# Kernel tuning notes

Hardware: AMD Instinct MI355X
Metric: run time of the kernel (lower is better)

The kernel has to match this reference:

```python
import jax, jax.numpy as jnp
import numpy as np

B, T, P, D, H = 4, 12, 196, 512, 8
DH = D // H
EPS = 1e-6


def _norm(x, alpha, bias):
    # torch Norm: alpha*(x-mean)/(std_unbiased+eps)+bias, std uses Bessel correction (ddof=1)
    mu = jnp.mean(x, axis=-1, keepdims=True)
    sd = jnp.std(x, axis=-1, ddof=1, keepdims=True)
    return alpha * (x - mu) / (sd + EPS) + bias


def setup_inputs() -> dict:
    key = jax.random.key(0)
    ks = jax.random.split(key, 12)
    s = 0.02

    def n(k, shape, scale=s):
        return jax.random.normal(k, shape, jnp.float32) * scale

    return {
        "x": jax.random.normal(ks[0], (B, T, P, D), jnp.float32),
        "Wq": n(ks[1], (D, D)), "bq": jnp.zeros((D,), jnp.float32),
        "Wk": n(ks[2], (D, D)), "bk": jnp.zeros((D,), jnp.float32),
        "Wv": n(ks[3], (D, D)), "bv": jnp.zeros((D,), jnp.float32),
        "in_a": jnp.ones((D,), jnp.float32), "in_b": jnp.zeros((D,), jnp.float32),
        "attn_a": jnp.ones((D,), jnp.float32), "attn_b": jnp.zeros((D,), jnp.float32),
        "out_a": jnp.ones((D,), jnp.float32), "out_b": jnp.zeros((D,), jnp.float32),
        "Wt": n(ks[4], (T, D, D)), "bt": jnp.zeros((T, D), jnp.float32),
        "pos": n(ks[5], (T, T, P, D), 0.02),
        "W1": n(ks[6], (2 * D, D)), "b1": jnp.zeros((2 * D,), jnp.float32),
        "W2": n(ks[7], (D, 2 * D)), "b2": jnp.zeros((D,), jnp.float32),
    }


def reference(x, Wq, bq, Wk, bk, Wv, bv, in_a, in_b, attn_a, attn_b,
              out_a, out_b, Wt, bt, pos, W1, b1, W2, b2):
    x2 = _norm(x, in_a, in_b)

    def proj(W, b):
        # [B,T,P,D] -> [B,T,H,P,DH]
        return (x2 @ W.T + b).reshape(B, T, P, H, DH).transpose(0, 1, 3, 2, 4)

    Q = proj(Wq, bq)
    K = proj(Wk, bk)
    V = proj(Wv, bv)

    # all-pairs temporal cross attention: [B,t,u,H,Pq,Pk]
    qk = jnp.einsum('btijk,builk->btuijl', Q, K) / np.sqrt(DH)
    attn = jax.nn.softmax(qk, axis=-1)  # no mask, dropout=0
    av = jnp.einsum('btuijl,builk->btuijk', attn, V)  # [B,t,u,H,P,DH]
    av = av.transpose(0, 1, 2, 4, 3, 5).reshape(B, T, T, P, D)
    av = _norm(av, attn_a, attn_b)
    x2p = av + pos  # pos broadcasts over batch

    # per-u Linear fused as one batched contraction, summed over u
    tc = jnp.einsum('btupd,ued->btpe', x2p / T, Wt) + jnp.sum(bt, axis=0)
    x = x + jax.nn.gelu(tc, approximate=False)

    x2 = _norm(x, out_a, out_b)
    h = jax.nn.gelu(x2 @ W1.T + b1, approximate=False)
    y = jax.nn.gelu(h @ W2.T + b2, approximate=False)
    return x + y
```

## Files before the change

### kernel.cpp

```cpp
#include <hip/hip_runtime.h>
#include <hip/hip_bf16.h>

typedef __hip_bfloat16 bf16;

typedef __bf16 bfrag8 __attribute__((ext_vector_type(8)));
typedef __bf16 bfrag4 __attribute__((ext_vector_type(4)));
typedef float  ffrag4 __attribute__((ext_vector_type(4)));
typedef float  ffrag16 __attribute__((ext_vector_type(16)));

#define EPS 1e-6f

__device__ __forceinline__ float gelu_exact(float v) {
  return 0.5f * v * (1.0f + erff(v * 0.7071067811865475f));
}

__device__ __forceinline__ void async16(const void* g, void* s) {
  __builtin_amdgcn_global_load_lds(
      (const __attribute__((address_space(1))) unsigned int*)g,
      (__attribute__((address_space(3))) unsigned int*)s, 16, 0, 0);
}

__device__ __forceinline__ int cvt_pk_bf16(float a, float b) {
  int r;
  asm("v_cvt_pk_bf16_f32 %0, %1, %2" : "=v"(r) : "v"(a), "v"(b));
  return r;
}
__device__ __forceinline__ void perm_swap(int& a, int& b) {
  asm volatile("v_permlane32_swap_b32 %0, %1" : "+v"(a), "+v"(b));
}

struct alignas(16) bf16x8 { bf16 v[8]; };
struct alignas(4)  bf16p2 { __bf16 v[2]; };

__global__ __launch_bounds__(256) void conv_w_kernel(
    const float* __restrict__ Wq, const float* __restrict__ Wk,
    const float* __restrict__ Wv, const float* __restrict__ W1,
    const float* __restrict__ W2, const float* __restrict__ Wt,
    __bf16* __restrict__ dst)
{
  size_t e = ((size_t)blockIdx.x * 256 + threadIdx.x) * 8;
  const float* src; size_t off, dsto;
  if      (e <  262144) { src = Wq; off = e;           dsto = e; }
  else if (e <  524288) { src = Wk; off = e -  262144; dsto = e; }
  else if (e <  786432) { src = Wv; off = e -  524288; dsto = e; }
  else if (e < 1310720) { src = W1; off = e -  786432; dsto = e; }
  else if (e < 1835008) { src = W2; off = e - 1310720; dsto = e; }
  else if (e < 4980736) {
    src = Wt; off = e - 1835008;
    size_t u = off >> 18;
    size_t rem = off & 262143;
    size_t eo = rem >> 9, d = rem & 511;
    dsto = 1835008 + eo * 6144 + u * 512 + d;
  }
  else return;
  float4 f0 = *(const float4*)(src + off);
  float4 f1 = *(const float4*)(src + off + 4);
  bfrag8 o;
  o[0] = (__bf16)f0.x; o[1] = (__bf16)f0.y; o[2] = (__bf16)f0.z; o[3] = (__bf16)f0.w;
  o[4] = (__bf16)f1.x; o[5] = (__bf16)f1.y; o[6] = (__bf16)f1.z; o[7] = (__bf16)f1.w;
  *(bfrag8*)(dst + dsto) = o;
}

__global__ __launch_bounds__(512) void sum_bt_kernel(
    const float* __restrict__ bt, float* __restrict__ sbt)
{
  int n = threadIdx.x;
  float s = 0.f;
#pragma unroll
  for (int u = 0; u < 12; ++u) s += bt[u * 512 + n];
  sbt[n] = s;
}

__global__ __launch_bounds__(64) void norm_f32_to_bf16_kernel(
    const float* __restrict__ in, __bf16* __restrict__ out,
    const float* __restrict__ alpha, const float* __restrict__ beta)
{
  size_t row = blockIdx.x;
  int l = threadIdx.x;
  const float* r = in + row * 512 + l * 8;
  float4 v0 = *(const float4*)(r);
  float4 v1 = *(const float4*)(r + 4);
  float f[8] = {v0.x, v0.y, v0.z, v0.w, v1.x, v1.y, v1.z, v1.w};
  float s = 0.f, ss = 0.f;
#pragma unroll
  for (int q = 0; q < 8; ++q) { s += f[q]; ss += f[q] * f[q]; }
#pragma unroll
  for (int off = 32; off; off >>= 1) { s += __shfl_xor(s, off); ss += __shfl_xor(ss, off); }
  float mu = s * (1.f / 512.f);
  float var = fmaxf((ss - 512.f * mu * mu) * (1.f / 511.f), 0.f);
  float inv = 1.f / (sqrtf(var) + EPS);
  const float* al = alpha + l * 8;
  const float* be = beta + l * 8;
  float4 a0 = *(const float4*)al, a1 = *(const float4*)(al + 4);
  float4 b0 = *(const float4*)be, b1 = *(const float4*)(be + 4);
  float aa[8] = {a0.x, a0.y, a0.z, a0.w, a1.x, a1.y, a1.z, a1.w};
  float bb[8] = {b0.x, b0.y, b0.z, b0.w, b1.x, b1.y, b1.z, b1.w};
  bfrag8 o;
#pragma unroll
  for (int q = 0; q < 8; ++q) o[q] = (__bf16)(aa[q] * (f[q] - mu) * inv + bb[q]);
  *(bfrag8*)(out + row * 512 + l * 8) = o;
}

__global__ __launch_bounds__(256) void norm_av_kernel(
    bf16* __restrict__ av, const float* __restrict__ alpha,
    const float* __restrict__ beta, const float* __restrict__ pos)
{
  size_t row = (size_t)blockIdx.x * 4 + (threadIdx.x >> 6);
  int l = threadIdx.x & 63;
  bf16* r = av + row * 512 + (size_t)l * 8;
  bf16x8 ib = *(const bf16x8*)r;
  float f[8];
#pragma unroll
  for (int q = 0; q < 8; ++q) f[q] = __bfloat162float(ib.v[q]);
  float s = 0.f, ss = 0.f;
#pragma unroll
  for (int q = 0; q < 8; ++q) { s += f[q]; ss += f[q] * f[q]; }
#pragma unroll
  for (int off = 32; off; off >>= 1) { s += __shfl_xor(s, off); ss += __shfl_xor(ss, off); }
  float mu = s * (1.f / 512.f);
  float var = fmaxf((ss - 512.f * mu * mu) * (1.f / 511.f), 0.f);
  float inv = 1.f / (sqrtf(var) + EPS);
  size_t prow = row % 28224;
  const float* pr = pos + prow * 512 + l * 8;
  float4 p0 = *(const float4*)pr, p1 = *(const float4*)(pr + 4);
  const float* al = alpha + l * 8;
  const float* be = beta + l * 8;
  float4 a0 = *(const float4*)al, a1 = *(const float4*)(al + 4);
  float4 b0 = *(const float4*)be, b1 = *(const float4*)(be + 4);
  float pa[8] = {p0.x, p0.y, p0.z, p0.w, p1.x, p1.y, p1.z, p1.w};
  float aa[8] = {a0.x, a0.y, a0.z, a0.w, a1.x, a1.y, a1.z, a1.w};
  float bb[8] = {b0.x, b0.y, b0.z, b0.w, b1.x, b1.y, b1.z, b1.w};
  bf16x8 ob;
#pragma unroll
  for (int q = 0; q < 8; ++q)
    ob.v[q] = __float2bfloat16(aa[q] * (f[q] - mu) * inv + bb[q] + pa[q]);
  *(bf16x8*)r = ob;
}

__global__ __launch_bounds__(256) void mfma_nt_kernel(
    const __bf16* __restrict__ A,
    const __bf16* __restrict__ Bq, const __bf16* __restrict__ Bk,
    const __bf16* __restrict__ Bv,
    const float* __restrict__ bq, const float* __restrict__ bk,
    const float* __restrict__ bv,
    __bf16* __restrict__ oq, __bf16* __restrict__ ok, __bf16* __restrict__ ov,
    const float* __restrict__ res, float* __restrict__ fout,
    int K, int mode)
{
  __shared__ __bf16 As[3 * 128 * 32];
  __shared__ __bf16 Bs[3 * 128 * 32];
  int tid = threadIdx.x;

  int nwg = gridDim.x * gridDim.y;
  int cpx = nwg >> 3;
  int lid = blockIdx.x + gridDim.x * blockIdx.y;
  int logical = (lid & 7) * cpx + (lid >> 3);
  int bx = logical % gridDim.x;
  int by = logical / gridDim.x;
  int m0 = by * 128;
  int n0g = bx * 128;

  const __bf16* Bsel; const float* biassel; __bf16* osel; int ncol0;
  if (mode == 0) {
    int sel = n0g >> 9;
    Bsel = sel == 0 ? Bq : (sel == 1 ? Bk : Bv);
    biassel = sel == 0 ? bq : (sel == 1 ? bk : bv);
    osel = sel == 0 ? oq : (sel == 1 ? ok : ov);
    ncol0 = n0g & 511;
  } else {
    Bsel = Bq; biassel = bq; osel = oq; ncol0 = n0g;
  }

  int srow = tid >> 2;
  int scol = ((tid & 3) ^ ((srow >> 1) & 3)) * 8;
  int rg0 = m0 + srow;       if (rg0 > 9407) rg0 = 9407;
  int rg1 = m0 + 64 + srow;  if (rg1 > 9407) rg1 = 9407;
  const __bf16* a0 = A + (size_t)rg0 * K + scol;
  const __bf16* a1 = A + (size_t)rg1 * K + scol;
  const __bf16* b0 = Bsel + (size_t)(ncol0 + srow) * K + scol;
  const __bf16* b1 = Bsel + (size_t)(ncol0 + 64 + srow) * K + scol;
  char* sa0 = (char*)As + tid * 16;
  char* sa1 = (char*)As + 4096 + tid * 16;
  char* sb0 = (char*)Bs + tid * 16;
  char* sb1 = (char*)Bs + 4096 + tid * 16;

  int l = tid & 63, w = tid >> 6;
  int lm = l & 15, lq = l >> 4;
  int wm = w >> 1, wn = w & 1;
  int rsw = ((((lm >> 1) & 3) ^ lq)) * 8;

  const int nsteps = K >> 5;
  async16(a0, sa0); async16(a1, sa1);
  async16(b0, sb0); async16(b1, sb1);
  async16(a0 + 32, sa0 + 8192); async16(a1 + 32, sa1 + 8192);
  async16(b0 + 32, sb0 + 8192); async16(b1 + 32, sb1 + 8192);
  __builtin_amdgcn_sched_barrier(0);
  asm volatile("s_waitcnt vmcnt(4)" ::: "memory");
  __builtin_amdgcn_s_barrier();
  __builtin_amdgcn_sched_barrier(0);

  ffrag4 acc[4][4] = {};
  int cur = 0;
  for (int t = 0; t < nsteps; ++t) {
    if (t + 2 < nsteps) {
      int k2 = (t + 2) << 5;
      int nb = cur + 2; if (nb >= 3) nb -= 3;
      int bo = nb * 8192;
      async16(a0 + k2, sa0 + bo); async16(a1 + k2, sa1 + bo);
      async16(b0 + k2, sb0 + bo); async16(b1 + k2, sb1 + bo);
    }
    int co = cur * 4096;
    bfrag8 af[4], bfr[4];
#pragma unroll
    for (int i = 0; i < 4; ++i)
      af[i] = *(const bfrag8*)&As[co + (wm * 64 + i * 16 + lm) * 32 + rsw];
#pragma unroll
    for (int j = 0; j < 4; ++j)
      bfr[j] = *(const bfrag8*)&Bs[co + (wn * 64 + j * 16 + lm) * 32 + rsw];
#pragma unroll
    for (int i = 0; i < 4; ++i)
#pragma unroll
      for (int j = 0; j < 4; ++j)
        acc[i][j] = __builtin_amdgcn_mfma_f32_16x16x32_bf16(af[i], bfr[j], acc[i][j], 0, 0, 0);
    __builtin_amdgcn_sched_barrier(0);
    if (t + 2 < nsteps) asm volatile("s_waitcnt vmcnt(4)" ::: "memory");
    else                asm volatile("s_waitcnt vmcnt(0)" ::: "memory");
    __builtin_amdgcn_s_barrier();
    __builtin_amdgcn_sched_barrier(0);
    cur += 1; if (cur == 3) cur = 0;
  }

#pragma unroll
  for (int i = 0; i < 4; ++i) {
    int mbase = m0 + wm * 64 + i * 16 + lq * 4;
#pragma unroll
    for (int j = 0; j < 4; ++j) {
      int n = ncol0 + wn * 64 + j * 16 + lm;
      float bj = biassel[n];
#pragma unroll
      for (int r = 0; r < 4; ++r) {
        int mr = mbase + r;
        if (mr < 9408) {
          float v = acc[i][j][r] + bj;
          if (mode == 0)      osel[(size_t)mr * 512 + n] = (__bf16)v;
          else if (mode == 1) osel[(size_t)mr * 1024 + n] = (__bf16)gelu_exact(v);
          else                fout[(size_t)mr * 512 + n] =
                                res[(size_t)mr * 512 + n] + gelu_exact(v);
        }
      }
    }
  }
}

__global__ __launch_bounds__(256) void mfma_tc_kernel(
    const __bf16* __restrict__ X2p, const __bf16* __restrict__ Wte,
    float* __restrict__ acc0, float* __restrict__ acc1)
{
  __shared__ __bf16 As[3 * 128 * 32];
  __shared__ __bf16 Bs[3 * 128 * 32];
  int tid = threadIdx.x;

  int lid = blockIdx.x + 4 * (blockIdx.y + 74 * blockIdx.z);
  int logical = (lid & 7) * 74 + (lid >> 3);
  int lx = logical & 3;
  int rest = logical >> 2;
  int ly = rest % 74;
  int lz = rest / 74;

  int m0 = ly * 128;
  int n0 = lx * 128;
  int kbeg = lz * 3072;
  float* accp = lz == 0 ? acc0 : acc1;

  int srow = tid >> 2;
  int scol = ((tid & 3) ^ ((srow >> 1) & 3)) * 8;
  int rg0 = m0 + srow;       if (rg0 > 9407) rg0 = 9407;
  int rg1 = m0 + 64 + srow;  if (rg1 > 9407) rg1 = 9407;
  int btq0 = rg0 / 196, p0_ = rg0 - btq0 * 196;
  int btq1 = rg1 / 196, p1_ = rg1 - btq1 * 196;
  const __bf16* a0 = X2p + (size_t)btq0 * 1204224 + (size_t)p0_ * 512 + scol;
  const __bf16* a1 = X2p + (size_t)btq1 * 1204224 + (size_t)p1_ * 512 + scol;
  const __bf16* b0 = Wte + (size_t)(n0 + srow) * 6144 + scol;
  const __bf16* b1 = Wte + (size_t)(n0 + 64 + srow) * 6144 + scol;
  char* sa0 = (char*)As + tid * 16;
  char* sa1 = (char*)As + 4096 + tid * 16;
  char* sb0 = (char*)Bs + tid * 16;
  char* sb1 = (char*)Bs + 4096 + tid * 16;

  int l = tid & 63, w = tid >> 6;
  int lm = l & 15, lq = l >> 4;
  int wm = w >> 1, wn = w & 1;
  int rsw = ((((lm >> 1) & 3) ^ lq)) * 8;

  {
    size_t ao0 = (size_t)(kbeg >> 9) * 100352 + (size_t)(kbeg & 511);
    int k1 = kbeg + 32;
    size_t ao1 = (size_t)(k1 >> 9) * 100352 + (size_t)(k1 & 511);
    async16(a0 + ao0, sa0); async16(a1 + ao0, sa1);
    async16(b0 + kbeg, sb0); async16(b1 + kbeg, sb1);
    async16(a0 + ao1, sa0 + 8192); async16(a1 + ao1, sa1 + 8192);
    async16(b0 + k1, sb0 + 8192); async16(b1 + k1, sb1 + 8192);
  }
  __builtin_amdgcn_sched_barrier(0);
  asm volatile("s_waitcnt vmcnt(4)" ::: "memory");
  __builtin_amdgcn_s_barrier();
  __builtin_amdgcn_sched_barrier(0);

  ffrag4 acc[4][4] = {};
  int cur = 0;
  for (int t = 0; t < 96; ++t) {
    if (t + 2 < 96) {
      int k2 = kbeg + (t + 2) * 32;
      size_t aoff = (size_t)(k2 >> 9) * 100352 + (size_t)(k2 & 511);
      int nb = cur + 2; if (nb >= 3) nb -= 3;
      int bo = nb * 8192;
      async16(a0 + aoff, sa0 + bo); async16(a1 + aoff, sa1 + bo);
      async16(b0 + k2, sb0 + bo); async16(b1 + k2, sb1 + bo);
    }
    int co = cur * 4096;
    bfrag8 af[4], bfr[4];
#pragma unroll
    for (int i = 0; i < 4; ++i)
      af[i] = *(const bfrag8*)&As[co + (wm * 64 + i * 16 + lm) * 32 + rsw];
#pragma unroll
    for (int j = 0; j < 4; ++j)
      bfr[j] = *(const bfrag8*)&Bs[co + (wn * 64 + j * 16 + lm) * 32 + rsw];
#pragma unroll
    for (int i = 0; i < 4; ++i)
#pragma unroll
      for (int j = 0; j < 4; ++j)
        acc[i][j] = __builtin_amdgcn_mfma_f32_16x16x32_bf16(af[i], bfr[j], acc[i][j], 0, 0, 0);
    __builtin_amdgcn_sched_barrier(0);
    if (t + 2 < 96) asm volatile("s_waitcnt vmcnt(4)" ::: "memory");
    else            asm volatile("s_waitcnt vmcnt(0)" ::: "memory");
    __builtin_amdgcn_s_barrier();
    __builtin_amdgcn_sched_barrier(0);
    cur += 1; if (cur == 3) cur = 0;
  }

#pragma unroll
  for (int i = 0; i < 4; ++i) {
    int mbase = m0 + wm * 64 + i * 16 + lq * 4;
#pragma unroll
    for (int j = 0; j < 4; ++j) {
      int n = n0 + wn * 64 + j * 16 + lm;
#pragma unroll
      for (int r = 0; r < 4; ++r) {
        int mr = mbase + r;
        if (mr < 9408)
          accp[(size_t)mr * 512 + n] = acc[i][j][r];
      }
    }
  }
}

__global__ __launch_bounds__(64) void tc_epi_norm_kernel(
    const float* __restrict__ acc0, const float* __restrict__ acc1,
    const float* __restrict__ x, const float* __restrict__ sbt,
    const float* __restrict__ alpha, const float* __restrict__ beta,
    float* __restrict__ xmid, __bf16* __restrict__ x3b)
{
  size_t row = blockIdx.x;
  int l = threadIdx.x;
  size_t base = row * 512 + l * 8;
  float4 c0 = *(const float4*)(acc0 + base);
  float4 c1 = *(const float4*)(acc0 + base + 4);
  float4 d0 = *(const float4*)(acc1 + base);
  float4 d1 = *(const float4*)(acc1 + base + 4);
  float4 x0 = *(const float4*)(x + base);
  float4 x1 = *(const float4*)(x + base + 4);
  float4 s0 = *(const float4*)(sbt + l * 8);
  float4 s1 = *(const float4*)(sbt + l * 8 + 4);
  float cc[8] = {c0.x + d0.x, c0.y + d0.y, c0.z + d0.z, c0.w + d0.w,
                 c1.x + d1.x, c1.y + d1.y, c1.z + d1.z, c1.w + d1.w};
  float xx[8] = {x0.x, x0.y, x0.z, x0.w, x1.x, x1.y, x1.z, x1.w};
  float sv[8] = {s0.x, s0.y, s0.z, s0.w, s1.x, s1.y, s1.z, s1.w};
  float f[8];
#pragma unroll
  for (int q = 0; q < 8; ++q)
    f[q] = xx[q] + gelu_exact(cc[q] * (1.f / 12.f) + sv[q]);
  *(float4*)(xmid + base)     = make_float4(f[0], f[1], f[2], f[3]);
  *(float4*)(xmid + base + 4) = make_float4(f[4], f[5], f[6], f[7]);
  float s = 0.f, ss = 0.f;
#pragma unroll
  for (int q = 0; q < 8; ++q) { s += f[q]; ss += f[q] * f[q]; }
#pragma unroll
  for (int off = 32; off; off >>= 1) { s += __shfl_xor(s, off); ss += __shfl_xor(ss, off); }
  float mu = s * (1.f / 512.f);
  float var = fmaxf((ss - 512.f * mu * mu) * (1.f / 511.f), 0.f);
  float inv = 1.f / (sqrtf(var) + EPS);
  const float* al = alpha + l * 8;
  const float* be = beta + l * 8;
  float4 a0 = *(const float4*)al, a1 = *(const float4*)(al + 4);
  float4 b0 = *(const float4*)be, b1 = *(const float4*)(be + 4);
  float aa[8] = {a0.x, a0.y, a0.z, a0.w, a1.x, a1.y, a1.z, a1.w};
  float bb[8] = {b0.x, b0.y, b0.z, b0.w, b1.x, b1.y, b1.z, b1.w};
  bfrag8 o;
#pragma unroll
  for (int q = 0; q < 8; ++q) o[q] = (__bf16)(aa[q] * (f[q] - mu) * inv + bb[q]);
  *(bfrag8*)(x3b + base) = o;
}

__global__ __launch_bounds__(512, 4) void attn_kernel(
    const __bf16* __restrict__ Q, const __bf16* __restrict__ K,
    const __bf16* __restrict__ V, __bf16* __restrict__ av)
{
  __shared__ __bf16 Ks[196 * 64];
  __shared__ __bf16 Vt[64 * 208];

  int bid = blockIdx.x;
  int half = bid & 1;
  int h = (bid >> 1) & 7;
  int r0 = bid >> 4;
  int u = r0 % 12;
  int b = r0 / 12;

  const __bf16* Kp = K + ((size_t)(b * 12 + u) * 196) * 512 + h * 64;
  const __bf16* Vp = V + ((size_t)(b * 12 + u) * 196) * 512 + h * 64;

  for (int idx = threadIdx.x; idx < 196 * 8; idx += 512) {
    int r = idx >> 3, g = idx & 7;
    *(bfrag8*)&Ks[r * 64 + ((g ^ (r & 7)) * 8)] =
        *(const bfrag8*)&Kp[(size_t)r * 512 + g * 8];
  }
  for (int idx = threadIdx.x; idx < 64 * 6; idx += 512) {
    int r = idx / 6, c2 = 196 + (idx % 6) * 2;
    bf16p2 z; z.v[0] = (__bf16)0.f; z.v[1] = (__bf16)0.f;
    *(bf16p2*)&Vt[r * 208 + c2] = z;
  }
  for (int idx = threadIdx.x; idx < 98 * 8; idx += 512) {
    int r2 = (idx % 98) * 2, c8 = (idx / 98) * 8;
    bfrag8 va = *(const bfrag8*)&Vp[(size_t)r2 * 512 + c8];
    bfrag8 vb = *(const bfrag8*)&Vp[(size_t)(r2 + 1) * 512 + c8];
#pragma unroll
    for (int e = 0; e < 8; ++e) {
      bf16p2 pr; pr.v[0] = va[e]; pr.v[1] = vb[e];
      *(bf16p2*)&Vt[(c8 + e) * 208 + r2] = pr;
    }
  }
  __syncthreads();

  int w = threadIdx.x >> 6, l = threadIdx.x & 63;
  int l5 = l >> 5, c = l & 31;

  for (int unit = w; unit < 42; unit += 8) {
    int t = unit / 7, qt = unit - t * 7;
    int tq = half * 6 + t;
    const __bf16* Qp = Q + ((size_t)(b * 12 + tq) * 196) * 512 + h * 64;
    __bf16* avp = av + ((size_t)((b * 12 + tq) * 12 + u) * 196) * 512 + h * 64;
    int q0 = qt * 32;

    const __bf16* qp = Qp + (size_t)(q0 + c) * 512 + l5 * 8;
    bfrag8 qf[4];
    qf[0] = *(const bfrag8*)(qp);
    qf[1] = *(const bfrag8*)(qp + 16);
    qf[2] = *(const bfrag8*)(qp + 32);
    qf[3] = *(const bfrag8*)(qp + 48);

    ffrag16 O0, O1;
#pragma unroll
    for (int g = 0; g < 16; ++g) { O0[g] = 0.f; O1[g] = 0.f; }
    float sumacc = 0.f;

    for (int nt = 0; nt < 6; ++nt) {
      int key = nt * 32 + c;
      const __bf16* kbase = &Ks[key * 64];
      int kx = key & 7;

      ffrag16 s;
#pragma unroll
      for (int g = 0; g < 16; ++g) s[g] = 0.f;
#pragma unroll
      for (int kc = 0; kc < 4; ++kc) {
        bfrag8 kf = *(const bfrag8*)&kbase[(((kc * 2 + l5) ^ kx) * 8)];
        s = __builtin_amdgcn_mfma_f32_32x32x16_bf16(kf, qf[kc], s, 0, 0, 0);
      }

#pragma unroll
      for (int g = 0; g < 16; ++g) {
        float e = __expf(s[g] * 0.125f);
        s[g] = e;
        sumacc += e;
      }

#pragma unroll
      for (int sub = 0; sub < 2; ++sub) {
        int A0 = cvt_pk_bf16(s[sub * 8 + 0], s[sub * 8 + 1]);
        int A1 = cvt_pk_bf16(s[sub * 8 + 2], s[sub * 8 + 3]);
        int A2 = cvt_pk_bf16(s[sub * 8 + 4], s[sub * 8 + 5]);
        int A3 = cvt_pk_bf16(s[sub * 8 + 6], s[sub * 8 + 7]);
        perm_swap(A0, A2);
        perm_swap(A1, A3);
        union { int i[4]; bfrag8 v; } pu;
        pu.i[0] = A0; pu.i[1] = A1; pu.i[2] = A2; pu.i[3] = A3;
        bfrag8 pa = pu.v;
        int ch = nt * 2 + sub;
        bfrag8 v0 = *(const bfrag8*)&Vt[(size_t)(c     ) * 208 + ch * 16 + l5 * 8];
        bfrag8 v1 = *(const bfrag8*)&Vt[(size_t)(c + 32) * 208 + ch * 16 + l5 * 8];
        O0 = __builtin_amdgcn_mfma_f32_32x32x16_bf16(pa, v0, O0, 0, 0, 0);
        O1 = __builtin_amdgcn_mfma_f32_32x32x16_bf16(pa, v1, O1, 0, 0, 0);
      }
    }

    {
      int key = 192 + c; if (key > 195) key = 195;
      const __bf16* kbase = &Ks[key * 64];
      int kx = key & 7;

      ffrag16 s;
#pragma unroll
      for (int g = 0; g < 16; ++g) s[g] = 0.f;
#pragma unroll
      for (int kc = 0; kc < 4; ++kc) {
        bfrag8 kf = *(const bfrag8*)&kbase[(((kc * 2 + l5) ^ kx) * 8)];
        s = __builtin_amdgcn_mfma_f32_32x32x16_bf16(kf, qf[kc], s, 0, 0, 0);
      }
#pragma unroll
      for (int g = 0; g < 16; ++g) {
        float e = __expf(s[g] * 0.125f);
        bool keep = (g < 4) && (l5 == 0);
        e = keep ? e : 0.f;
        s[g] = e;
        sumacc += e;
      }
      int A0 = cvt_pk_bf16(s[0], s[1]);
      int A1 = cvt_pk_bf16(s[2], s[3]);
      int A2 = cvt_pk_bf16(s[4], s[5]);
      int A3 = cvt_pk_bf16(s[6], s[7]);
      perm_swap(A0, A2);
      perm_swap(A1, A3);
      union { int i[4]; bfrag8 v; } pu;
      pu.i[0] = A0; pu.i[1] = A1; pu.i[2] = A2; pu.i[3] = A3;
      bfrag8 pa = pu.v;
      bfrag8 v0 = *(const bfrag8*)&Vt[(size_t)(c     ) * 208 + 12 * 16 + l5 * 8];
      bfrag8 v1 = *(const bfrag8*)&Vt[(size_t)(c + 32) * 208 + 12 * 16 + l5 * 8];
      O0 = __builtin_amdgcn_mfma_f32_32x32x16_bf16(pa, v0, O0, 0, 0, 0);
      O1 = __builtin_amdgcn_mfma_f32_32x32x16_bf16(pa, v1, O1, 0, 0, 0);
    }

    float stot = sumacc + __shfl_xor(sumacc, 32);

#pragma unroll
    for (int g = 0; g < 16; ++g) {
      int row = (g & 3) + 8 * (g >> 2) + 4 * l5;
      float sq = __shfl(stot, row);
      float iv = __builtin_amdgcn_rcpf(sq);
      int q = q0 + row;
      if (q < 196) {
        size_t base = (size_t)q * 512 + c;
        avp[base]      = (__bf16)(O0[g] * iv);
        avp[base + 32] = (__bf16)(O1[g] * iv);
      }
    }
  }
}

extern "C" void kernel_launch(void* const* d_in, const int* in_sizes, int n_in,
                              void* d_out, int out_size, void* d_ws, size_t ws_size,
                              hipStream_t stream)
{
  const float* x      = (const float*)d_in[0];
  const float* Wq     = (const float*)d_in[1];
  const float* bq     = (const float*)d_in[2];
  const float* Wk     = (const float*)d_in[3];
  const float* bk     = (const float*)d_in[4];
  const float* Wv     = (const float*)d_in[5];
  const float* bv     = (const float*)d_in[6];
  const float* in_a   = (const float*)d_in[7];
  const float* in_b   = (const float*)d_in[8];
  const float* attn_a = (const float*)d_in[9];
  const float* attn_b = (const float*)d_in[10];
  const float* out_a  = (const float*)d_in[11];
  const float* out_b  = (const float*)d_in[12];
  const float* Wt     = (const float*)d_in[13];
  const float* bt     = (const float*)d_in[14];
  const float* pos    = (const float*)d_in[15];
  const float* W1     = (const float*)d_in[16];
  const float* b1     = (const float*)d_in[17];
  const float* W2     = (const float*)d_in[18];
  const float* b2     = (const float*)d_in[19];

  char* ws = (char*)d_ws;
  const size_t bfb = (size_t)9408 * 512 * 2;
  __bf16* x2b  = (__bf16*)(ws);
  __bf16* Qb   = (__bf16*)(ws + bfb);
  __bf16* Kb   = (__bf16*)(ws + 2 * bfb);
  __bf16* Vb   = (__bf16*)(ws + 3 * bfb);
  __bf16* av   = (__bf16*)(ws + 4 * bfb);
  char*   wreg = ws + 4 * bfb + (size_t)115605504;
  __bf16* Wqb  = (__bf16*)(wreg);
  __bf16* Wkb  = (__bf16*)(wreg) + 262144;
  __bf16* Wvb  = (__bf16*)(wreg) + 524288;
  __bf16* W1b  = (__bf16*)(wreg) + 786432;
  __bf16* W2b  = (__bf16*)(wreg) + 1310720;
  __bf16* Wtb  = (__bf16*)(wreg) + 1835008;
  float*  sbt  = (float*)(wreg + 9961472);
  float*  acc0 = (float*)(wreg + 9963520);
  float*  acc1 = (float*)(ws + 2 * bfb);
  float*  xmid = (float*)(ws);
  __bf16* x3b  = (__bf16*)(ws + 4 * bfb + 33554432);
  __bf16* hb   = (__bf16*)(ws + 4 * bfb);
  float*  out  = (float*)d_out;

  conv_w_kernel<<<2432, 256, 0, stream>>>(Wq, Wk, Wv, W1, W2, Wt, (__bf16*)wreg);
  sum_bt_kernel<<<1, 512, 0, stream>>>(bt, sbt);
  norm_f32_to_bf16_kernel<<<9408, 64, 0, stream>>>(x, x2b, in_a, in_b);
  mfma_nt_kernel<<<dim3(12, 74), 256, 0, stream>>>(
      x2b, Wqb, Wkb, Wvb, bq, bk, bv, Qb, Kb, Vb, nullptr, nullptr, 512, 0);
  attn_kernel<<<768, 512, 0, stream>>>(Qb, Kb, Vb, av);
  norm_av_kernel<<<28224, 256, 0, stream>>>((bf16*)av, attn_a, attn_b, pos);
  mfma_tc_kernel<<<dim3(4, 74, 2), 256, 0, stream>>>(av, Wtb, acc0, acc1);
  tc_epi_norm_kernel<<<9408, 64, 0, stream>>>(acc0, acc1, x, sbt, out_a, out_b, xmid, x3b);
  mfma_nt_kernel<<<dim3(8, 74), 256, 0, stream>>>(
      x3b, W1b, nullptr, nullptr, b1, nullptr, nullptr, hb, nullptr, nullptr,
      nullptr, nullptr, 512, 1);
  mfma_nt_kernel<<<dim3(4, 74), 256, 0, stream>>>(
      hb, W2b, nullptr, nullptr, b2, nullptr, nullptr, nullptr, nullptr, nullptr,
      xmid, out, 1024, 2);
}
```

Measured before the change: 510.3 us.

## Split GEMM tiles across 8 waves and raise MFMA priority in attention

The QKV, temporal-contraction and MLP GEMM kernels now launch 512 threads per block instead of 256. Each 128x128 tile is shared by 8 waves that each hold 32x64 accumulators. Each thread issues one A and one B async load per stage, with the vmcnt waits adjusted to match. The aim is more waves to hide latency and lower accumulator register pressure per wave, at the cost of more barrier participants and less fragment reuse per wave. Separately, the attention kernel wraps its MFMA sequences in s_setprio to favour matrix-issue waves over softmax work.

```diff
diff --git a/kernel.cpp b/kernel.cpp
--- a/kernel.cpp
+++ b/kernel.cpp
@@ -137,7 +137,7 @@
   *(bf16x8*)r = ob;
 }
 
-__global__ __launch_bounds__(256) void mfma_nt_kernel(
+__global__ __launch_bounds__(512) void mfma_nt_kernel(
     const __bf16* __restrict__ A,
     const __bf16* __restrict__ Bq, const __bf16* __restrict__ Bk,
     const __bf16* __restrict__ Bv,
@@ -174,15 +174,10 @@
   int srow = tid >> 2;
   int scol = ((tid & 3) ^ ((srow >> 1) & 3)) * 8;
   int rg0 = m0 + srow;       if (rg0 > 9407) rg0 = 9407;
-  int rg1 = m0 + 64 + srow;  if (rg1 > 9407) rg1 = 9407;
   const __bf16* a0 = A + (size_t)rg0 * K + scol;
-  const __bf16* a1 = A + (size_t)rg1 * K + scol;
   const __bf16* b0 = Bsel + (size_t)(ncol0 + srow) * K + scol;
-  const __bf16* b1 = Bsel + (size_t)(ncol0 + 64 + srow) * K + scol;
   char* sa0 = (char*)As + tid * 16;
-  char* sa1 = (char*)As + 4096 + tid * 16;
   char* sb0 = (char*)Bs + tid * 16;
-  char* sb1 = (char*)Bs + 4096 + tid * 16;
 
   int l = tid & 63, w = tid >> 6;
   int lm = l & 15, lq = l >> 4;
@@ -190,40 +185,37 @@
   int rsw = ((((lm >> 1) & 3) ^ lq)) * 8;
 
   const int nsteps = K >> 5;
-  async16(a0, sa0); async16(a1, sa1);
-  async16(b0, sb0); async16(b1, sb1);
-  async16(a0 + 32, sa0 + 8192); async16(a1 + 32, sa1 + 8192);
-  async16(b0 + 32, sb0 + 8192); async16(b1 + 32, sb1 + 8192);
+  async16(a0, sa0); async16(b0, sb0);
+  async16(a0 + 32, sa0 + 8192); async16(b0 + 32, sb0 + 8192);
   __builtin_amdgcn_sched_barrier(0);
-  asm volatile("s_waitcnt vmcnt(4)" ::: "memory");
+  asm volatile("s_waitcnt vmcnt(2)" ::: "memory");
   __builtin_amdgcn_s_barrier();
   __builtin_amdgcn_sched_barrier(0);
 
-  ffrag4 acc[4][4] = {};
+  ffrag4 acc[2][4] = {};
   int cur = 0;
   for (int t = 0; t < nsteps; ++t) {
     if (t + 2 < nsteps) {
       int k2 = (t + 2) << 5;
       int nb = cur + 2; if (nb >= 3) nb -= 3;
       int bo = nb * 8192;
-      async16(a0 + k2, sa0 + bo); async16(a1 + k2, sa1 + bo);
-      async16(b0 + k2, sb0 + bo); async16(b1 + k2, sb1 + bo);
+      async16(a0 + k2, sa0 + bo); async16(b0 + k2, sb0 + bo);
     }
     int co = cur * 4096;
-    bfrag8 af[4], bfr[4];
-#pragma unroll
-    for (int i = 0; i < 4; ++i)
-      af[i] = *(const bfrag8*)&As[co + (wm * 64 + i * 16 + lm) * 32 + rsw];
+    bfrag8 af[2], bfr[4];
+#pragma unroll
+    for (int i = 0; i < 2; ++i)
+      af[i] = *(const bfrag8*)&As[co + (wm * 32 + i * 16 + lm) * 32 + rsw];
 #pragma unroll
     for (int j = 0; j < 4; ++j)
       bfr[j] = *(const bfrag8*)&Bs[co + (wn * 64 + j * 16 + lm) * 32 + rsw];
 #pragma unroll
-    for (int i = 0; i < 4; ++i)
+    for (int i = 0; i < 2; ++i)
 #pragma unroll
       for (int j = 0; j < 4; ++j)
         acc[i][j] = __builtin_amdgcn_mfma_f32_16x16x32_bf16(af[i], bfr[j], acc[i][j], 0, 0, 0);
     __builtin_amdgcn_sched_barrier(0);
-    if (t + 2 < nsteps) asm volatile("s_waitcnt vmcnt(4)" ::: "memory");
+    if (t + 2 < nsteps) asm volatile("s_waitcnt vmcnt(2)" ::: "memory");
     else                asm volatile("s_waitcnt vmcnt(0)" ::: "memory");
     __builtin_amdgcn_s_barrier();
     __builtin_amdgcn_sched_barrier(0);
@@ -231,8 +223,8 @@
   }
 
 #pragma unroll
-  for (int i = 0; i < 4; ++i) {
-    int mbase = m0 + wm * 64 + i * 16 + lq * 4;
+  for (int i = 0; i < 2; ++i) {
+    int mbase = m0 + wm * 32 + i * 16 + lq * 4;
 #pragma unroll
     for (int j = 0; j < 4; ++j) {
       int n = ncol0 + wn * 64 + j * 16 + lm;
@@ -252,7 +244,7 @@
   }
 }
 
-__global__ __launch_bounds__(256) void mfma_tc_kernel(
+__global__ __launch_bounds__(512) void mfma_tc_kernel(
     const __bf16* __restrict__ X2p, const __bf16* __restrict__ Wte,
     float* __restrict__ acc0, float* __restrict__ acc1)
 {
@@ -275,17 +267,11 @@
   int srow = tid >> 2;
   int scol = ((tid & 3) ^ ((srow >> 1) & 3)) * 8;
   int rg0 = m0 + srow;       if (rg0 > 9407) rg0 = 9407;
-  int rg1 = m0 + 64 + srow;  if (rg1 > 9407) rg1 = 9407;
   int btq0 = rg0 / 196, p0_ = rg0 - btq0 * 196;
-  int btq1 = rg1 / 196, p1_ = rg1 - btq1 * 196;
   const __bf16* a0 = X2p + (size_t)btq0 * 1204224 + (size_t)p0_ * 512 + scol;
-  const __bf16* a1 = X2p + (size_t)btq1 * 1204224 + (size_t)p1_ * 512 + scol;
   const __bf16* b0 = Wte + (size_t)(n0 + srow) * 6144 + scol;
-  const __bf16* b1 = Wte + (size_t)(n0 + 64 + srow) * 6144 + scol;
   char* sa0 = (char*)As + tid * 16;
-  char* sa1 = (char*)As + 4096 + tid * 16;
   char* sb0 = (char*)Bs + tid * 16;
-  char* sb1 = (char*)Bs + 4096 + tid * 16;
 
   int l = tid & 63, w = tid >> 6;
   int lm = l & 15, lq = l >> 4;
@@ -296,17 +282,15 @@
     size_t ao0 = (size_t)(kbeg >> 9) * 100352 + (size_t)(kbeg & 511);
     int k1 = kbeg + 32;
     size_t ao1 = (size_t)(k1 >> 9) * 100352 + (size_t)(k1 & 511);
-    async16(a0 + ao0, sa0); async16(a1 + ao0, sa1);
-    async16(b0 + kbeg, sb0); async16(b1 + kbeg, sb1);
-    async16(a0 + ao1, sa0 + 8192); async16(a1 + ao1, sa1 + 8192);
-    async16(b0 + k1, sb0 + 8192); async16(b1 + k1, sb1 + 8192);
+    async16(a0 + ao0, sa0); async16(b0 + kbeg, sb0);
+    async16(a0 + ao1, sa0 + 8192); async16(b0 + k1, sb0 + 8192);
   }
   __builtin_amdgcn_sched_barrier(0);
-  asm volatile("s_waitcnt vmcnt(4)" ::: "memory");
+  asm volatile("s_waitcnt vmcnt(2)" ::: "memory");
   __builtin_amdgcn_s_barrier();
   __builtin_amdgcn_sched_barrier(0);
 
-  ffrag4 acc[4][4] = {};
+  ffrag4 acc[2][4] = {};
   int cur = 0;
   for (int t = 0; t < 96; ++t) {
     if (t + 2 < 96) {
@@ -314,24 +298,23 @@
       size_t aoff = (size_t)(k2 >> 9) * 100352 + (size_t)(k2 & 511);
       int nb = cur + 2; if (nb >= 3) nb -= 3;
       int bo = nb * 8192;
-      async16(a0 + aoff, sa0 + bo); async16(a1 + aoff, sa1 + bo);
-      async16(b0 + k2, sb0 + bo); async16(b1 + k2, sb1 + bo);
+      async16(a0 + aoff, sa0 + bo); async16(b0 + k2, sb0 + bo);
     }
     int co = cur * 4096;
-    bfrag8 af[4], bfr[4];
-#pragma unroll
-    for (int i = 0; i < 4; ++i)
-      af[i] = *(const bfrag8*)&As[co + (wm * 64 + i * 16 + lm) * 32 + rsw];
+    bfrag8 af[2], bfr[4];
+#pragma unroll
+    for (int i = 0; i < 2; ++i)
+      af[i] = *(const bfrag8*)&As[co + (wm * 32 + i * 16 + lm) * 32 + rsw];
 #pragma unroll
     for (int j = 0; j < 4; ++j)
       bfr[j] = *(const bfrag8*)&Bs[co + (wn * 64 + j * 16 + lm) * 32 + rsw];
 #pragma unroll
-    for (int i = 0; i < 4; ++i)
+    for (int i = 0; i < 2; ++i)
 #pragma unroll
       for (int j = 0; j < 4; ++j)
         acc[i][j] = __builtin_amdgcn_mfma_f32_16x16x32_bf16(af[i], bfr[j], acc[i][j], 0, 0, 0);
     __builtin_amdgcn_sched_barrier(0);
-    if (t + 2 < 96) asm volatile("s_waitcnt vmcnt(4)" ::: "memory");
+    if (t + 2 < 96) asm volatile("s_waitcnt vmcnt(2)" ::: "memory");
     else            asm volatile("s_waitcnt vmcnt(0)" ::: "memory");
     __builtin_amdgcn_s_barrier();
     __builtin_amdgcn_sched_barrier(0);
@@ -339,8 +322,8 @@
   }
 
 #pragma unroll
-  for (int i = 0; i < 4; ++i) {
-    int mbase = m0 + wm * 64 + i * 16 + lq * 4;
+  for (int i = 0; i < 2; ++i) {
+    int mbase = m0 + wm * 32 + i * 16 + lq * 4;
 #pragma unroll
     for (int j = 0; j < 4; ++j) {
       int n = n0 + wn * 64 + j * 16 + lm;
@@ -470,11 +453,13 @@
       ffrag16 s;
 #pragma unroll
       for (int g = 0; g < 16; ++g) s[g] = 0.f;
+      __builtin_amdgcn_s_setprio(1);
 #pragma unroll
       for (int kc = 0; kc < 4; ++kc) {
         bfrag8 kf = *(const bfrag8*)&kbase[(((kc * 2 + l5) ^ kx) * 8)];
         s = __builtin_amdgcn_mfma_f32_32x32x16_bf16(kf, qf[kc], s, 0, 0, 0);
       }
+      __builtin_amdgcn_s_setprio(0);
 
 #pragma unroll
       for (int g = 0; g < 16; ++g) {
@@ -497,8 +482,10 @@
         int ch = nt * 2 + sub;
         bfrag8 v0 = *(const bfrag8*)&Vt[(size_t)(c     ) * 208 + ch * 16 + l5 * 8];
         bfrag8 v1 = *(const bfrag8*)&Vt[(size_t)(c + 32) * 208 + ch * 16 + l5 * 8];
+        __builtin_amdgcn_s_setprio(1);
         O0 = __builtin_amdgcn_mfma_f32_32x32x16_bf16(pa, v0, O0, 0, 0, 0);
         O1 = __builtin_amdgcn_mfma_f32_32x32x16_bf16(pa, v1, O1, 0, 0, 0);
+        __builtin_amdgcn_s_setprio(0);
       }
     }
 
@@ -510,11 +497,13 @@
       ffrag16 s;
 #pragma unroll
       for (int g = 0; g < 16; ++g) s[g] = 0.f;
+      __builtin_amdgcn_s_setprio(1);
 #pragma unroll
       for (int kc = 0; kc < 4; ++kc) {
         bfrag8 kf = *(const bfrag8*)&kbase[(((kc * 2 + l5) ^ kx) * 8)];
         s = __builtin_amdgcn_mfma_f32_32x32x16_bf16(kf, qf[kc], s, 0, 0, 0);
       }
+      __builtin_amdgcn_s_setprio(0);
 #pragma unroll
       for (int g = 0; g < 16; ++g) {
         float e = __expf(s[g] * 0.125f);
@@ -534,8 +523,10 @@
       bfrag8 pa = pu.v;
       bfrag8 v0 = *(const bfrag8*)&Vt[(size_t)(c     ) * 208 + 12 * 16 + l5 * 8];
       bfrag8 v1 = *(const bfrag8*)&Vt[(size_t)(c + 32) * 208 + 12 * 16 + l5 * 8];
+      __builtin_amdgcn_s_setprio(1);
       O0 = __builtin_amdgcn_mfma_f32_32x32x16_bf16(pa, v0, O0, 0, 0, 0);
       O1 = __builtin_amdgcn_mfma_f32_32x32x16_bf16(pa, v1, O1, 0, 0, 0);
+      __builtin_amdgcn_s_setprio(0);
     }
 
     float stot = sumacc + __shfl_xor(sumacc, 32);
@@ -605,16 +596,16 @@
   conv_w_kernel<<<2432, 256, 0, stream>>>(Wq, Wk, Wv, W1, W2, Wt, (__bf16*)wreg);
   sum_bt_kernel<<<1, 512, 0, stream>>>(bt, sbt);
   norm_f32_to_bf16_kernel<<<9408, 64, 0, stream>>>(x, x2b, in_a, in_b);
-  mfma_nt_kernel<<<dim3(12, 74), 256, 0, stream>>>(
+  mfma_nt_kernel<<<dim3(12, 74), 512, 0, stream>>>(
       x2b, Wqb, Wkb, Wvb, bq, bk, bv, Qb, Kb, Vb, nullptr, nullptr, 512, 0);
   attn_kernel<<<768, 512, 0, stream>>>(Qb, Kb, Vb, av);
   norm_av_kernel<<<28224, 256, 0, stream>>>((bf16*)av, attn_a, attn_b, pos);
-  mfma_tc_kernel<<<dim3(4, 74, 2), 256, 0, stream>>>(av, Wtb, acc0, acc1);
+  mfma_tc_kernel<<<dim3(4, 74, 2), 512, 0, stream>>>(av, Wtb, acc0, acc1);
   tc_epi_norm_kernel<<<9408, 64, 0, stream>>>(acc0, acc1, x, sbt, out_a, out_b, xmid, x3b);
-  mfma_nt_kernel<<<dim3(8, 74), 256, 0, stream>>>(
+  mfma_nt_kernel<<<dim3(8, 74), 512, 0, stream>>>(
       x3b, W1b, nullptr, nullptr, b1, nullptr, nullptr, hb, nullptr, nullptr,
       nullptr, nullptr, 512, 1);
-  mfma_nt_kernel<<<dim3(4, 74), 256, 0, stream>>>(
+  mfma_nt_kernel<<<dim3(4, 74), 512, 0, stream>>>(
       hb, W2b, nullptr, nullptr, b2, nullptr, nullptr, nullptr, nullptr, nullptr,
       xmid, out, 1024, 2);
 }
```

Result: faster. 469.0 us (-8.1%).
